# Optimization experiments

Measured on AMD Instinct MI355X. Metric: run time of the kernel, lower is better.

## Reference

```python
import jax, jax.numpy as jnp
import numpy as np

H, F, K, R = 8, 64, 10, 256  # num_heads, in_features, num_sines, num_realizations
B, L = 4, 2048


def setup_inputs() -> dict:
    key = jax.random.key(0)
    k1, k2, k3, k4, k5, k6 = jax.random.split(key, 6)
    return {
        "queries": jax.random.normal(k1, (B, L, H, F), dtype=jnp.float32),
        "keys": jax.random.normal(k2, (B, L, H, F), dtype=jnp.float32),
        "z": jax.random.normal(k3, (B, H, F, 2 * K, R), dtype=jnp.float32),
        "freqs": jax.random.normal(k4, (H, F, K), dtype=jnp.float32),
        "offsets": jax.random.normal(k5, (H, F, K), dtype=jnp.float32),
        "gains": jax.random.normal(k6, (H, F, K), dtype=jnp.float32),
    }


def reference(queries, keys, z, freqs, offsets, gains):
    h, f_dim, k_sines = freqs.shape
    length = queries.shape[1]
    r = z.shape[-1]
    # split positional / non-positional features (rest is empty here: key_dim == in_features)
    q_pos, q_rest = queries[..., :f_dim], queries[..., f_dim:]
    k_pos, k_rest = keys[..., :f_dim], keys[..., f_dim:]

    idx = jnp.arange(length, dtype=queries.dtype)  # linspace(0, L-1, L)
    fr = jax.nn.sigmoid(freqs)[:, :, None, :] / 2.0          # [H, F, 1, K]
    base = 2.0 * jnp.pi * fr * idx[None, None, :, None]       # [H, F, L, K]
    ph_q = base + offsets[:, :, None, :]
    ph_k = base
    # stack(cos, sin) on last axis then flatten -> interleaved cos0,sin0,... : [H, F, L, 2K]
    omega_q = jnp.stack([jnp.cos(ph_q), jnp.sin(ph_q)], axis=-1).reshape(h, f_dim, length, 2 * k_sines)
    omega_k = jnp.stack([jnp.cos(ph_k), jnp.sin(ph_k)], axis=-1).reshape(h, f_dim, length, 2 * k_sines)

    g = jnp.tile(jax.nn.softplus(gains), (1, 1, 2))           # [H, F, 2K] (block-repeated, as in torch .repeat)
    zs = z * g[None, :, :, :, None] / np.sqrt(r * f_dim).astype(np.float32)  # [B, H, F, 2K, R]

    # fused double contraction over f (in_features) and s (2K sines); equals
    # (omega @ z) permuted then multiplied by queries and summed over in_features
    qhat = jnp.einsum('hfls,bhfsr,blhf->blhr', omega_q, zs, q_pos)  # [B, L, H, R]
    khat = jnp.einsum('hfls,bhfsr,blhf->blhr', omega_k, zs, k_pos)

    qhat = jnp.concatenate([qhat, q_rest], axis=-1)
    khat = jnp.concatenate([khat, k_rest], axis=-1)
    return qhat, khat
```

## Files before the change

### kernel.cpp

```cpp
#include <hip/hip_runtime.h>
#include <math.h>


#define NH 8
#define NF 64
#define NK 10
#define NR 256
#define NB 4
#define NL 2048
#define KTOT 1280
#define BK 32
#define NCH (KTOT/BK)
#define NFRAG_B 16
#define WS_NEEDED ((size_t)NB*NH*NCH*NFRAG_B*1024)

typedef __attribute__((ext_vector_type(8))) short short8;
typedef __attribute__((ext_vector_type(4))) float f32x4;
typedef __attribute__((ext_vector_type(4))) unsigned int u32x4;
typedef __attribute__((ext_vector_type(2))) unsigned int u32x2;

static __device__ __forceinline__ unsigned short f2b(float f) {
    unsigned x = __float_as_uint(f);
    return (unsigned short)((x + 0x7FFFu + ((x >> 16) & 1u)) >> 16);
}
static __device__ __forceinline__ unsigned int pk2(float a, float b) {
    return (unsigned int)f2b(a) | ((unsigned int)f2b(b) << 16);
}
static __device__ __forceinline__ unsigned int cvtpk(float lo, float hi) {
    unsigned int r;
    asm("v_cvt_pk_bf16_f32 %0, %1, %2" : "=v"(r) : "v"(lo), "v"(hi));
    return r;
}
static __device__ __forceinline__ void gload_lds16(const void* g, void* l) {
    __builtin_amdgcn_global_load_lds(
        (const __attribute__((address_space(1))) unsigned int*)g,
        (__attribute__((address_space(3))) unsigned int*)l, 16, 0, 0);
}

__global__ __launch_bounds__(256)
void spe_prep(const float* __restrict__ z, const float* __restrict__ gains,
              unsigned char* __restrict__ bpack)
{
    __shared__ float s_g[NF*NK];
    const int ch  = blockIdx.x;
    const int bh  = blockIdx.y;
    const int h   = bh & 7;
    const int tid = threadIdx.x;
    for (int i = tid; i < NF*NK; i += 256)
        s_g[i] = log1pf(expf(gains[h*NF*NK + i])) * 0.0078125f;
    __syncthreads();
    const float* zb = z + (size_t)bh * KTOT * NR;
    unsigned char* dst = bpack + ((size_t)(bh*NCH + ch) * NFRAG_B) * 1024;
    #pragma unroll
    for (int it = 0; it < 4; ++it) {
        const int s  = tid + 256*it;
        const int fi = s >> 6;
        const int l  = s & 63;
        const int r  = fi*16 + (l & 15);
        const int k0 = ch*BK + (l >> 4)*8;
        u32x4 wv;
        #pragma unroll
        for (int jp = 0; jp < 4; ++jp) {
            const int ka = k0 + 2*jp, kb = ka + 1;
            const int fa = (ka*3277) >> 16; int sa = ka - fa*20; if (sa >= NK) sa -= NK;
            const int fb = (kb*3277) >> 16; int sb = kb - fb*20; if (sb >= NK) sb -= NK;
            const float va = zb[(size_t)ka*NR + r] * s_g[fa*NK + sa];
            const float vb = zb[(size_t)kb*NR + r] * s_g[fb*NK + sb];
            wv[jp] = pk2(va, vb);
        }
        *(u32x4*)(dst + (size_t)s*16) = wv;
    }
}

#define OFF_B   0
#define OFF_A   49152
#define OFF_POS 57344
#define OFF_FR  73728
#define OFF_CO  76288
#define OFF_SO  78848
#define SMEM_SZ 81408

__global__ __launch_bounds__(512, 4)
void spe_main(const float* __restrict__ queries, const float* __restrict__ keys,
              const float* __restrict__ freqs, const float* __restrict__ offsets,
              const unsigned char* __restrict__ bpack, float* __restrict__ out)
{
    __shared__ __attribute__((aligned(16))) unsigned char smem[SMEM_SZ];
    const int tid  = threadIdx.x;
    const int lane = tid & 63;
    const int w    = tid >> 6;
    const int l0   = blockIdx.x * 64;
    const int bh   = blockIdx.y;
    const int b = bh >> 3, h = bh & 7;

    float* ld_fr = (float*)(smem + OFF_FR);
    float* ld_co = (float*)(smem + OFF_CO);
    float* ld_so = (float*)(smem + OFF_SO);
    unsigned short* pos_t = (unsigned short*)(smem + OFF_POS);

    for (int i = tid; i < NF*NK; i += 512) {
        const float fv = freqs[h*NF*NK + i];
        ld_fr[i] = 0.5f / (1.0f + expf(-fv));
        const float xo = __builtin_amdgcn_fractf(offsets[h*NF*NK + i] * 0.15915494309189535f);
        ld_co[i] = __builtin_amdgcn_cosf(xo);
        ld_so[i] = __builtin_amdgcn_sinf(xo);
    }
    {
        const int r  = tid >> 2;
        const int f0 = (tid & 3) * 16;
        const int rl = r & 63;
        const float* src = (r < 64)
            ? queries + ((size_t)((b*NL + l0 + rl)*NH + h))*NF + f0
            : keys    + ((size_t)((b*NL + l0 + rl)*NH + h))*NF + f0;
        unsigned short* pdst = pos_t + ((r >> 6) << 12);
        #pragma unroll
        for (int j = 0; j < 4; ++j) {
            const float4 v = *(const float4*)(src + j*4);
            const int f = f0 + j*4;
            pdst[(f+0)*64 + rl] = f2b(v.x);
            pdst[(f+1)*64 + rl] = f2b(v.y);
            pdst[(f+2)*64 + rl] = f2b(v.z);
            pdst[(f+3)*64 + rl] = f2b(v.w);
        }
    }
    __syncthreads();

    const unsigned char* bp = bpack + (size_t)bh * ((size_t)NCH*NFRAG_B*1024);
    const int fi0 = w*2;
    gload_lds16(bp + (size_t)fi0*1024 + lane*16,                 smem + OFF_B + (fi0  <<10));
    gload_lds16(bp + (size_t)(fi0+1)*1024 + lane*16,             smem + OFF_B + ((fi0+1)<<10));
    gload_lds16(bp + (size_t)(NFRAG_B + fi0)*1024 + lane*16,     smem + OFF_B + 16384 + (fi0  <<10));
    gload_lds16(bp + (size_t)(NFRAG_B + fi0+1)*1024 + lane*16,   smem + OFF_B + 16384 + ((fi0+1)<<10));

    const int wm = w >> 2, wn = w & 3;
    f32x4 acc[4][4];
    #pragma unroll
    for (int mi = 0; mi < 4; ++mi)
        #pragma unroll
        for (int ni = 0; ni < 4; ++ni)
            acc[mi][ni] = (f32x4){0.f, 0.f, 0.f, 0.f};

    const int rq   = ((w & 1) << 5) | (lane & 31);
    const int oct  = w >> 1;
    const int half = lane >> 5;
    const float lf = (float)(l0 + rq);
    const unsigned short* posq = pos_t;
    const unsigned short* posk = pos_t + 4096;
    const int aw_q = OFF_A + ((rq >> 4) << 10) + ((oct*16 + (rq & 15)) << 4) + (half << 3);
    const int aw_k = aw_q + 4096;

    auto synthA = [&](int t, u32x2& q01, u32x2& k01) {
        #pragma unroll
        for (int p = 0; p < 2; ++p) {
            const int kk   = t*BK + oct*8 + half*4 + p*2;
            const int f    = (kk*3277) >> 16;
            const int srem = kk - f*20;
            const int kidx = f*NK + (srem >> 1);
            const float x  = __builtin_amdgcn_fractf(ld_fr[kidx] * lf);
            const float ck = __builtin_amdgcn_cosf(x);
            const float sk = __builtin_amdgcn_sinf(x);
            const float co = ld_co[kidx], so = ld_so[kidx];
            const float cq = ck*co - sk*so;
            const float sq = sk*co + ck*so;
            const float pq = __uint_as_float(((unsigned)posq[f*64 + rq]) << 16);
            const float pk = __uint_as_float(((unsigned)posk[f*64 + rq]) << 16);
            q01[p] = cvtpk(cq*pq, sq*pq);
            k01[p] = cvtpk(ck*pk, sk*pk);
        }
    };

    u32x2 q01, k01;
    synthA(0, q01, k01);

    int bsel  = 0;
    int bsel2 = 2;
    for (int t = 0; t < NCH; ++t) {
        if (t < NCH-1) { asm volatile("s_waitcnt vmcnt(2)" ::: "memory"); }
        else           { asm volatile("s_waitcnt vmcnt(0)" ::: "memory"); }
        __builtin_amdgcn_sched_barrier(0);
        __builtin_amdgcn_s_barrier();

        if (t + 2 < NCH) {
            unsigned char* Bn = smem + OFF_B + bsel2*16384;
            gload_lds16(bp + (size_t)((t+2)*NFRAG_B + fi0)*1024 + lane*16,
                        Bn + (fi0<<10));
            gload_lds16(bp + (size_t)((t+2)*NFRAG_B + fi0+1)*1024 + lane*16,
                        Bn + ((fi0+1)<<10));
        }

        *(u32x2*)(smem + aw_q) = q01;
        *(u32x2*)(smem + aw_k) = k01;
        asm volatile("s_waitcnt lgkmcnt(0)" ::: "memory");
        __builtin_amdgcn_sched_barrier(0);
        __builtin_amdgcn_s_barrier();

        const unsigned char* Bc = smem + OFF_B + bsel*16384;
        short8 bf[4];
        #pragma unroll
        for (int ni = 0; ni < 4; ++ni)
            bf[ni] = *(const short8*)(Bc + ((wn*4 + ni) << 10) + (lane << 4));

        if (t + 1 < NCH) synthA(t + 1, q01, k01);

        #pragma unroll
        for (int mi = 0; mi < 4; ++mi) {
            const short8 af = *(const short8*)(smem + OFF_A + ((wm*4 + mi) << 10) + (lane << 4));
            #pragma unroll
            for (int ni = 0; ni < 4; ++ni)
                acc[mi][ni] = __builtin_amdgcn_mfma_f32_16x16x32_bf16(af, bf[ni], acc[mi][ni], 0, 0, 0);
        }

        bsel  = (bsel  == 2) ? 0 : bsel  + 1;
        bsel2 = (bsel2 == 2) ? 0 : bsel2 + 1;
    }

    const size_t qk_off = (size_t)wm * ((size_t)NB*NL*NH*NR);
    const int row_l = (lane >> 4) * 4;
    const int col_r = lane & 15;
    #pragma unroll
    for (int mi = 0; mi < 4; ++mi) {
        const int lg = l0 + mi*16 + row_l;
        #pragma unroll
        for (int ni = 0; ni < 4; ++ni) {
            const int rg = wn*64 + ni*16 + col_r;
            const f32x4 v = acc[mi][ni];
            #pragma unroll
            for (int q = 0; q < 4; ++q)
                out[qk_off + ((size_t)((b*NL + lg + q)*NH + h))*NR + rg] = v[q];
        }
    }
}

#define BMF 128
#define FOFF_B   0
#define FOFF_A   32768
#define FOFF_POS 49152
#define FOFF_FR  65536
#define FOFF_OFS 68096
#define FOFF_GS  70656
#define FSMEM_SZ 73216

__global__ __launch_bounds__(512, 4)
void spe_mfma_fb(const float* __restrict__ queries, const float* __restrict__ keys,
                 const float* __restrict__ z, const float* __restrict__ freqs,
                 const float* __restrict__ offsets, const float* __restrict__ gains,
                 float* __restrict__ out)
{
    __shared__ __attribute__((aligned(16))) unsigned char smem[FSMEM_SZ];
    const int tid = threadIdx.x, lane = tid & 63;
    const int l0 = blockIdx.x * BMF, bh = blockIdx.y;
    const int b = bh >> 3, h = bh & 7, isK = blockIdx.z;
    float* ld_fr = (float*)(smem + FOFF_FR);
    float* ld_of = (float*)(smem + FOFF_OFS);
    float* ld_gs = (float*)(smem + FOFF_GS);
    unsigned short* pos_t = (unsigned short*)(smem + FOFF_POS);
    for (int i = tid; i < NF*NK; i += 512) {
        const float fv = freqs[h*NF*NK + i];
        ld_fr[i] = 0.5f / (1.0f + expf(-fv));
        ld_of[i] = isK ? 0.0f : offsets[h*NF*NK + i] * 0.15915494309189535f;
        ld_gs[i] = log1pf(expf(gains[h*NF*NK + i])) * 0.0078125f;
    }
    {
        const float* pos = isK ? keys : queries;
        #pragma unroll
        for (int i = 0; i < 4; ++i) {
            const int lrow = (tid >> 4) + 32*i;
            const int f0 = (tid & 15) * 4;
            const float4 v = *(const float4*)(pos + ((size_t)((b*NL + l0 + lrow)*NH + h))*NF + f0);
            pos_t[(f0+0)*BMF + lrow] = f2b(v.x); pos_t[(f0+1)*BMF + lrow] = f2b(v.y);
            pos_t[(f0+2)*BMF + lrow] = f2b(v.z); pos_t[(f0+3)*BMF + lrow] = f2b(v.w);
        }
    }
    __syncthreads();
    const int w = tid >> 6, wm = w >> 2, wn = w & 3;
    f32x4 acc[4][4];
    #pragma unroll
    for (int mi = 0; mi < 4; ++mi)
        #pragma unroll
        for (int ni = 0; ni < 4; ++ni) acc[mi][ni] = (f32x4){0.f,0.f,0.f,0.f};
    const float* zbh = z + (size_t)(b*NH + h) * ((size_t)KTOT*NR);
    for (int ch = 0; ch < KTOT/64; ++ch) {
        const int fs0 = ch * 64;
        #pragma unroll
        for (int i = 0; i < 4; ++i) {
            const int tau = tid + 512*i, r = tau & 255, krun = tau >> 8;
            const float* zp = zbh + (size_t)(fs0 + krun*8)*NR + r;
            u32x4 wv2;
            #pragma unroll
            for (int jp = 0; jp < 4; ++jp) {
                const int fs = fs0 + krun*8 + 2*jp;
                const int f = (fs*3277) >> 16; const int rem = fs - f*20;
                const int km = (rem >= NK) ? rem - NK : rem;
                const int kn = ((rem+1) >= NK && (rem+1) < 2*NK) ? rem+1-NK : rem+1;
                const float sc0 = ld_gs[f*NK + km], sc1 = ld_gs[f*NK + (kn < NK ? kn : kn-NK)];
                wv2[jp] = pk2(zp[(2*jp)*NR]*sc0, zp[(2*jp+1)*NR]*sc1);
            }
            *(u32x4*)(smem + FOFF_B + ((((krun>>2)*16) + (r>>4)) << 10)
                                    + ((((krun&3)*16) + (r&15)) << 4)) = wv2;
        }
        #pragma unroll
        for (int i = 0; i < 2; ++i) {
            const int tau = tid + 512*i, m = tau & 127, krun = tau >> 7;
            const float lff = (float)(l0 + m);
            u32x4 wv2;
            #pragma unroll
            for (int jp = 0; jp < 4; ++jp) {
                const int fs = fs0 + krun*8 + 2*jp;
                const int f = (fs*3277) >> 16; const int rem = fs - f*20;
                const int kidx = f*NK + (rem >> 1);
                const float x = __builtin_amdgcn_fractf(ld_of[kidx] + ld_fr[kidx]*lff);
                const float c = __builtin_amdgcn_cosf(x), sn = __builtin_amdgcn_sinf(x);
                const float p = __uint_as_float(((unsigned)pos_t[f*BMF + m]) << 16);
                wv2[jp] = pk2(c*p, sn*p);
            }
            *(u32x4*)(smem + FOFF_A + ((((krun>>2)*8) + (m>>4)) << 10)
                                    + ((((krun&3)*16) + (m&15)) << 4)) = wv2;
        }
        __syncthreads();
        #pragma unroll
        for (int ks = 0; ks < 2; ++ks) {
            short8 bf[4];
            #pragma unroll
            for (int ni = 0; ni < 4; ++ni)
                bf[ni] = *(const short8*)(smem + FOFF_B + ((ks*16 + wn*4 + ni) << 10) + (lane << 4));
            #pragma unroll
            for (int mi = 0; mi < 4; ++mi) {
                const short8 af = *(const short8*)(smem + FOFF_A + ((ks*8 + wm*4 + mi) << 10) + (lane << 4));
                #pragma unroll
                for (int ni = 0; ni < 4; ++ni)
                    acc[mi][ni] = __builtin_amdgcn_mfma_f32_16x16x32_bf16(af, bf[ni], acc[mi][ni], 0, 0, 0);
            }
        }
        __syncthreads();
    }
    const size_t qk_off = (size_t)isK * ((size_t)NB*NL*NH*NR);
    const int row_l = (lane >> 4) * 4, col_r = lane & 15;
    #pragma unroll
    for (int mi = 0; mi < 4; ++mi) {
        const int lg = l0 + wm*64 + mi*16 + row_l;
        #pragma unroll
        for (int ni = 0; ni < 4; ++ni) {
            const int rg = wn*64 + ni*16 + col_r;
            const f32x4 v = acc[mi][ni];
            #pragma unroll
            for (int q = 0; q < 4; ++q)
                out[qk_off + ((size_t)((b*NL + lg + q)*NH + h))*NR + rg] = v[q];
        }
    }
}

extern "C" void kernel_launch(void* const* d_in, const int* in_sizes, int n_in,
                              void* d_out, int out_size, void* d_ws, size_t ws_size,
                              hipStream_t stream) {
    const float* queries = (const float*)d_in[0];
    const float* keys    = (const float*)d_in[1];
    const float* z       = (const float*)d_in[2];
    const float* freqs   = (const float*)d_in[3];
    const float* offsets = (const float*)d_in[4];
    const float* gains   = (const float*)d_in[5];
    float* out = (float*)d_out;

    if (ws_size >= WS_NEEDED) {
        unsigned char* bpack = (unsigned char*)d_ws;
        spe_prep<<<dim3(NCH, NB*NH), 256, 0, stream>>>(z, gains, bpack);
        spe_main<<<dim3(NL/64, NB*NH), 512, 0, stream>>>(queries, keys, freqs, offsets, bpack, out);
    } else {
        spe_mfma_fb<<<dim3(NL/BMF, NB*NH, 2), 512, 0, stream>>>(queries, keys, z, freqs, offsets, gains, out);
    }
}
```

Measured before the change: 127.1 us.

## Precompute key-side trig table and pipeline main GEMM with triple-buffered B

After: 145.7 us. 1.15x slower.

```diff
diff --git a/kernel.cpp b/kernel.cpp
--- a/kernel.cpp
+++ b/kernel.cpp
@@ -12,7 +12,9 @@
 #define BK 32
 #define NCH (KTOT/BK)
 #define NFRAG_B 16
-#define WS_NEEDED ((size_t)NB*NH*NCH*NFRAG_B*1024)
+#define WS_BPACK ((size_t)NB*NH*NCH*NFRAG_B*1024)
+#define WS_TRIG  ((size_t)NH*NCH*2048*16*4)
+#define WS_NEED2 (WS_BPACK + WS_TRIG)
 
 typedef __attribute__((ext_vector_type(8))) short short8;
 typedef __attribute__((ext_vector_type(4))) float f32x4;
@@ -72,6 +74,190 @@
     }
 }
 
+__global__ __launch_bounds__(256)
+void spe_trig(const float* __restrict__ freqs, unsigned int* __restrict__ trig)
+{
+    const int t = blockIdx.x;
+    const int h = blockIdx.y;
+    const int tid = threadIdx.x;
+    #pragma unroll
+    for (int it = 0; it < 32; ++it) {
+        const int site = tid + 256*it;
+        const int l  = site >> 2;
+        const int jg = site & 3;
+        u32x4 wv;
+        #pragma unroll
+        for (int j = 0; j < 4; ++j) {
+            const int kidx2 = t*16 + jg*4 + j;
+            const float fv = freqs[h*640 + kidx2];
+            const float fr = 0.5f / (1.0f + expf(-fv));
+            const float x  = __builtin_amdgcn_fractf(fr * (float)l);
+            wv[j] = pk2(__builtin_amdgcn_cosf(x), __builtin_amdgcn_sinf(x));
+        }
+        *(u32x4*)(trig + ((size_t)(h*NCH + t)*2048 + l)*16 + jg*4) = wv;
+    }
+}
+
+#define OFF2_B   0
+#define OFF2_A   49152
+#define OFF2_POS 81920
+#define OFF2_CS  114688
+#define SMEM2_SZ 119808
+
+__global__ __launch_bounds__(1024, 4)
+void spe_main2(const float* __restrict__ queries, const float* __restrict__ keys,
+               const float* __restrict__ offsets,
+               const unsigned char* __restrict__ bpack,
+               const unsigned int* __restrict__ trig,
+               float* __restrict__ out)
+{
+    __shared__ __attribute__((aligned(16))) unsigned char smem[SMEM2_SZ];
+    const int tid  = threadIdx.x;
+    const int lane = tid & 63;
+    const int w    = tid >> 6;
+
+    const int bid = blockIdx.x;
+    const int swz = (bid & 7) * 64 + (bid >> 3);
+    const int l0  = (swz & 15) * 128;
+    const int bh  = swz >> 4;
+    const int b = bh >> 3, h = bh & 7;
+
+    float2* ld_cs = (float2*)(smem + OFF2_CS);
+    unsigned short* pos_t = (unsigned short*)(smem + OFF2_POS);
+
+    for (int i = tid; i < NF*NK; i += 1024) {
+        const float xo = __builtin_amdgcn_fractf(offsets[h*640 + i] * 0.15915494309189535f);
+        ld_cs[i] = make_float2(__builtin_amdgcn_cosf(xo), __builtin_amdgcn_sinf(xo));
+    }
+    {
+        const int row = tid & 127;
+        const int qk  = (tid >> 7) & 1;
+        const int fg  = tid >> 8;
+        const float* src = (qk ? keys : queries)
+            + ((size_t)((b*NL + l0 + row)*NH + h))*NF + fg*16;
+        unsigned short* pd = pos_t + qk*8192 + (fg*16)*128 + row;
+        #pragma unroll
+        for (int jj = 0; jj < 4; ++jj) {
+            const float4 v = *(const float4*)(src + jj*4);
+            pd[(jj*4+0)*128] = f2b(v.x);
+            pd[(jj*4+1)*128] = f2b(v.y);
+            pd[(jj*4+2)*128] = f2b(v.z);
+            pd[(jj*4+3)*128] = f2b(v.w);
+        }
+    }
+    __syncthreads();
+
+    const unsigned char* bp = bpack + (size_t)bh * ((size_t)NCH*NFRAG_B*1024);
+    const unsigned int*  tp = trig  + (size_t)h  * ((size_t)NCH*2048*16);
+
+    const int wq = w >> 2, wn = w & 3;
+    const int sqk  = w >> 3;
+    const int soct = (w >> 1) & 3;
+    const int srq  = ((w & 1) << 6) | lane;
+    const unsigned short* posm = pos_t + sqk*8192;
+    const int a_w = ((sqk*8 + (srq >> 4)) << 10) + ((soct*16 + (srq & 15)) << 4);
+    const size_t t_off = ((size_t)(l0 + srq))*16 + soct*4;
+
+    f32x4 acc[4][4];
+    #pragma unroll
+    for (int mi = 0; mi < 4; ++mi)
+        #pragma unroll
+        for (int ni = 0; ni < 4; ++ni)
+            acc[mi][ni] = (f32x4){0.f, 0.f, 0.f, 0.f};
+
+    u32x4 trA = *(const u32x4*)(tp + t_off);
+    gload_lds16(bp + (size_t)w*1024 + (size_t)lane*16, smem + OFF2_B + (w << 10));
+    u32x4 trB;
+
+    auto synthA = [&](int tt, const u32x4& tr, int apar) {
+        u32x4 av;
+        #pragma unroll
+        for (int p = 0; p < 4; ++p) {
+            const int kidx2 = tt*16 + soct*4 + p;
+            const int f = (kidx2 * 6554) >> 16;
+            const float ck = __uint_as_float(tr[p] << 16);
+            const float sk = __uint_as_float(tr[p] & 0xffff0000u);
+            const float pv = __uint_as_float(((unsigned)posm[f*128 + srq]) << 16);
+            float c, s;
+            if (sqk == 0) {
+                const float2 cs = ld_cs[kidx2];
+                c = ck*cs.x - sk*cs.y;
+                s = sk*cs.x + ck*cs.y;
+            } else { c = ck; s = sk; }
+            av[p] = cvtpk(c*pv, s*pv);
+        }
+        *(u32x4*)(smem + OFF2_A + apar*16384 + a_w) = av;
+    };
+
+    auto mfmaStep = [&](int bsel_, int apar) {
+        const unsigned char* Bc = smem + OFF2_B + bsel_*16384;
+        short8 bf[4];
+        #pragma unroll
+        for (int ni = 0; ni < 4; ++ni)
+            bf[ni] = *(const short8*)(Bc + ((wn*4 + ni) << 10) + (lane << 4));
+        const unsigned char* Ac = smem + OFF2_A + apar*16384;
+        #pragma unroll
+        for (int mi = 0; mi < 4; ++mi) {
+            const short8 af = *(const short8*)(Ac + ((wq*4 + mi) << 10) + (lane << 4));
+            #pragma unroll
+            for (int ni = 0; ni < 4; ++ni)
+                acc[mi][ni] = __builtin_amdgcn_mfma_f32_16x16x32_bf16(af, bf[ni], acc[mi][ni], 0, 0, 0);
+        }
+    };
+
+    int bsel = 0;
+    #pragma unroll 1
+    for (int t = 0; t < NCH; t += 2) {
+        {
+            const int tn = t + 1;
+            const int wb = (bsel + 1 == 3) ? 0 : bsel + 1;
+            trB = *(const u32x4*)(tp + (size_t)tn*2048*16 + t_off);
+            gload_lds16(bp + ((size_t)tn*NFRAG_B + w)*1024 + (size_t)lane*16,
+                        smem + OFF2_B + wb*16384 + (w << 10));
+            asm volatile("s_waitcnt vmcnt(2)" ::: "memory");
+            __builtin_amdgcn_sched_barrier(0);
+            synthA(t, trA, 0);
+            asm volatile("s_waitcnt lgkmcnt(0)" ::: "memory");
+            __builtin_amdgcn_sched_barrier(0);
+            __builtin_amdgcn_s_barrier();
+            mfmaStep(bsel, 0);
+            bsel = wb;
+        }
+        {
+            const int tn = (t + 2 < NCH) ? t + 2 : NCH - 1;
+            const int wb = (bsel + 1 == 3) ? 0 : bsel + 1;
+            trA = *(const u32x4*)(tp + (size_t)tn*2048*16 + t_off);
+            gload_lds16(bp + ((size_t)tn*NFRAG_B + w)*1024 + (size_t)lane*16,
+                        smem + OFF2_B + wb*16384 + (w << 10));
+            asm volatile("s_waitcnt vmcnt(2)" ::: "memory");
+            __builtin_amdgcn_sched_barrier(0);
+            synthA(t + 1, trB, 1);
+            asm volatile("s_waitcnt lgkmcnt(0)" ::: "memory");
+            __builtin_amdgcn_sched_barrier(0);
+            __builtin_amdgcn_s_barrier();
+            mfmaStep(bsel, 1);
+            bsel = wb;
+        }
+    }
+
+    const size_t qk_off = (size_t)(wq >> 1) * ((size_t)NB*NL*NH*NR);
+    const int mbase = l0 + (wq & 1) * 64;
+    const int row_l = (lane >> 4) * 4;
+    const int col_r = lane & 15;
+    #pragma unroll
+    for (int mi = 0; mi < 4; ++mi) {
+        const int lg = mbase + mi*16 + row_l;
+        #pragma unroll
+        for (int ni = 0; ni < 4; ++ni) {
+            const int rg = wn*64 + ni*16 + col_r;
+            const f32x4 v = acc[mi][ni];
+            #pragma unroll
+            for (int q = 0; q < 4; ++q)
+                out[qk_off + ((size_t)((b*NL + lg + q)*NH + h))*NR + rg] = v[q];
+        }
+    }
+}
+
 #define OFF_B   0
 #define OFF_A   49152
 #define OFF_POS 57344
@@ -127,10 +313,10 @@
 
     const unsigned char* bp = bpack + (size_t)bh * ((size_t)NCH*NFRAG_B*1024);
     const int fi0 = w*2;
-    gload_lds16(bp + (size_t)fi0*1024 + lane*16,                 smem + OFF_B + (fi0  <<10));
-    gload_lds16(bp + (size_t)(fi0+1)*1024 + lane*16,             smem + OFF_B + ((fi0+1)<<10));
-    gload_lds16(bp + (size_t)(NFRAG_B + fi0)*1024 + lane*16,     smem + OFF_B + 16384 + (fi0  <<10));
-    gload_lds16(bp + (size_t)(NFRAG_B + fi0+1)*1024 + lane*16,   smem + OFF_B + 16384 + ((fi0+1)<<10));
+    gload_lds16(bp + (size_t)fi0*1024 + lane*16,               smem + OFF_B + (fi0  <<10));
+    gload_lds16(bp + (size_t)(fi0+1)*1024 + lane*16,           smem + OFF_B + ((fi0+1)<<10));
+    gload_lds16(bp + (size_t)(NFRAG_B + fi0)*1024 + lane*16,   smem + OFF_B + 16384 + (fi0  <<10));
+    gload_lds16(bp + (size_t)(NFRAG_B + fi0+1)*1024 + lane*16, smem + OFF_B + 16384 + ((fi0+1)<<10));
 
     const int wm = w >> 2, wn = w & 3;
     f32x4 acc[4][4];
@@ -231,124 +417,6 @@
     }
 }
 
-#define BMF 128
-#define FOFF_B   0
-#define FOFF_A   32768
-#define FOFF_POS 49152
-#define FOFF_FR  65536
-#define FOFF_OFS 68096
-#define FOFF_GS  70656
-#define FSMEM_SZ 73216
-
-__global__ __launch_bounds__(512, 4)
-void spe_mfma_fb(const float* __restrict__ queries, const float* __restrict__ keys,
-                 const float* __restrict__ z, const float* __restrict__ freqs,
-                 const float* __restrict__ offsets, const float* __restrict__ gains,
-                 float* __restrict__ out)
-{
-    __shared__ __attribute__((aligned(16))) unsigned char smem[FSMEM_SZ];
-    const int tid = threadIdx.x, lane = tid & 63;
-    const int l0 = blockIdx.x * BMF, bh = blockIdx.y;
-    const int b = bh >> 3, h = bh & 7, isK = blockIdx.z;
-    float* ld_fr = (float*)(smem + FOFF_FR);
-    float* ld_of = (float*)(smem + FOFF_OFS);
-    float* ld_gs = (float*)(smem + FOFF_GS);
-    unsigned short* pos_t = (unsigned short*)(smem + FOFF_POS);
-    for (int i = tid; i < NF*NK; i += 512) {
-        const float fv = freqs[h*NF*NK + i];
-        ld_fr[i] = 0.5f / (1.0f + expf(-fv));
-        ld_of[i] = isK ? 0.0f : offsets[h*NF*NK + i] * 0.15915494309189535f;
-        ld_gs[i] = log1pf(expf(gains[h*NF*NK + i])) * 0.0078125f;
-    }
-    {
-        const float* pos = isK ? keys : queries;
-        #pragma unroll
-        for (int i = 0; i < 4; ++i) {
-            const int lrow = (tid >> 4) + 32*i;
-            const int f0 = (tid & 15) * 4;
-            const float4 v = *(const float4*)(pos + ((size_t)((b*NL + l0 + lrow)*NH + h))*NF + f0);
-            pos_t[(f0+0)*BMF + lrow] = f2b(v.x); pos_t[(f0+1)*BMF + lrow] = f2b(v.y);
-            pos_t[(f0+2)*BMF + lrow] = f2b(v.z); pos_t[(f0+3)*BMF + lrow] = f2b(v.w);
-        }
-    }
-    __syncthreads();
-    const int w = tid >> 6, wm = w >> 2, wn = w & 3;
-    f32x4 acc[4][4];
-    #pragma unroll
-    for (int mi = 0; mi < 4; ++mi)
-        #pragma unroll
-        for (int ni = 0; ni < 4; ++ni) acc[mi][ni] = (f32x4){0.f,0.f,0.f,0.f};
-    const float* zbh = z + (size_t)(b*NH + h) * ((size_t)KTOT*NR);
-    for (int ch = 0; ch < KTOT/64; ++ch) {
-        const int fs0 = ch * 64;
-        #pragma unroll
-        for (int i = 0; i < 4; ++i) {
-            const int tau = tid + 512*i, r = tau & 255, krun = tau >> 8;
-            const float* zp = zbh + (size_t)(fs0 + krun*8)*NR + r;
-            u32x4 wv2;
-            #pragma unroll
-            for (int jp = 0; jp < 4; ++jp) {
-                const int fs = fs0 + krun*8 + 2*jp;
-                const int f = (fs*3277) >> 16; const int rem = fs - f*20;
-                const int km = (rem >= NK) ? rem - NK : rem;
-                const int kn = ((rem+1) >= NK && (rem+1) < 2*NK) ? rem+1-NK : rem+1;
-                const float sc0 = ld_gs[f*NK + km], sc1 = ld_gs[f*NK + (kn < NK ? kn : kn-NK)];
-                wv2[jp] = pk2(zp[(2*jp)*NR]*sc0, zp[(2*jp+1)*NR]*sc1);
-            }
-            *(u32x4*)(smem + FOFF_B + ((((krun>>2)*16) + (r>>4)) << 10)
-                                    + ((((krun&3)*16) + (r&15)) << 4)) = wv2;
-        }
-        #pragma unroll
-        for (int i = 0; i < 2; ++i) {
-            const int tau = tid + 512*i, m = tau & 127, krun = tau >> 7;
-            const float lff = (float)(l0 + m);
-            u32x4 wv2;
-            #pragma unroll
-            for (int jp = 0; jp < 4; ++jp) {
-                const int fs = fs0 + krun*8 + 2*jp;
-                const int f = (fs*3277) >> 16; const int rem = fs - f*20;
-                const int kidx = f*NK + (rem >> 1);
-                const float x = __builtin_amdgcn_fractf(ld_of[kidx] + ld_fr[kidx]*lff);
-                const float c = __builtin_amdgcn_cosf(x), sn = __builtin_amdgcn_sinf(x);
-                const float p = __uint_as_float(((unsigned)pos_t[f*BMF + m]) << 16);
-                wv2[jp] = pk2(c*p, sn*p);
-            }
-            *(u32x4*)(smem + FOFF_A + ((((krun>>2)*8) + (m>>4)) << 10)
-                                    + ((((krun&3)*16) + (m&15)) << 4)) = wv2;
-        }
-        __syncthreads();
-        #pragma unroll
-        for (int ks = 0; ks < 2; ++ks) {
-            short8 bf[4];
-            #pragma unroll
-            for (int ni = 0; ni < 4; ++ni)
-                bf[ni] = *(const short8*)(smem + FOFF_B + ((ks*16 + wn*4 + ni) << 10) + (lane << 4));
-            #pragma unroll
-            for (int mi = 0; mi < 4; ++mi) {
-                const short8 af = *(const short8*)(smem + FOFF_A + ((ks*8 + wm*4 + mi) << 10) + (lane << 4));
-                #pragma unroll
-                for (int ni = 0; ni < 4; ++ni)
-                    acc[mi][ni] = __builtin_amdgcn_mfma_f32_16x16x32_bf16(af, bf[ni], acc[mi][ni], 0, 0, 0);
-            }
-        }
-        __syncthreads();
-    }
-    const size_t qk_off = (size_t)isK * ((size_t)NB*NL*NH*NR);
-    const int row_l = (lane >> 4) * 4, col_r = lane & 15;
-    #pragma unroll
-    for (int mi = 0; mi < 4; ++mi) {
-        const int lg = l0 + wm*64 + mi*16 + row_l;
-        #pragma unroll
-        for (int ni = 0; ni < 4; ++ni) {
-            const int rg = wn*64 + ni*16 + col_r;
-            const f32x4 v = acc[mi][ni];
-            #pragma unroll
-            for (int q = 0; q < 4; ++q)
-                out[qk_off + ((size_t)((b*NL + lg + q)*NH + h))*NR + rg] = v[q];
-        }
-    }
-}
-
 extern "C" void kernel_launch(void* const* d_in, const int* in_sizes, int n_in,
                               void* d_out, int out_size, void* d_ws, size_t ws_size,
                               hipStream_t stream) {
@@ -360,11 +428,14 @@
     const float* gains   = (const float*)d_in[5];
     float* out = (float*)d_out;
 
-    if (ws_size >= WS_NEEDED) {
-        unsigned char* bpack = (unsigned char*)d_ws;
-        spe_prep<<<dim3(NCH, NB*NH), 256, 0, stream>>>(z, gains, bpack);
+    unsigned char* bpack = (unsigned char*)d_ws;
+    spe_prep<<<dim3(NCH, NB*NH), 256, 0, stream>>>(z, gains, bpack);
+
+    if (ws_size >= WS_NEED2) {
+        unsigned int* trig = (unsigned int*)(bpack + WS_BPACK);
+        spe_trig<<<dim3(NCH, NH), 256, 0, stream>>>(freqs, trig);
+        spe_main2<<<dim3(512), 1024, 0, stream>>>(queries, keys, offsets, bpack, trig, out);
+    } else {
         spe_main<<<dim3(NL/64, NB*NH), 512, 0, stream>>>(queries, keys, freqs, offsets, bpack, out);
-    } else {
-        spe_mfma_fb<<<dim3(NL/BMF, NB*NH, 2), 512, 0, stream>>>(queries, keys, z, freqs, offsets, gains, out);
-    }
-}
+    }
+}
```
